# Performance work log

Hardware: AMD Instinct MI355X
Metric: run time of the kernel (lower is better)

Reference implementation:

```python
import jax, jax.numpy as jnp
import numpy as np
from jax import lax

EPS = 1e-5

def _bn(x):
    # BatchNorm1d, training-mode batch stats, affine at init (gamma=1, beta=0)
    return (x - x.mean(0)) / jnp.sqrt(x.var(0) + EPS)

def _nonlinear(x, W1, W2):
    h = jax.nn.relu(_bn(x @ W1.T))
    return jax.nn.relu(_bn(h @ W2.T))

def _conv_bn_lrelu(x, w):
    # x: [E, C, L], w: [O, C, 3], padding=1; BN over (batch, length)
    y = lax.conv_general_dilated(x, w, (1,), [(1, 1)], dimension_numbers=('NCH', 'OIH', 'NCH'))
    m = y.mean((0, 2), keepdims=True)
    v = y.var((0, 2), keepdims=True)
    y = (y - m) / jnp.sqrt(v + EPS)
    return jnp.where(y >= 0, y, 0.01 * y)  # LeakyReLU(negative_slope=0.01)

def _curve_encoder(x, c1, c2, c3, fc):
    y = _conv_bn_lrelu(x, c1)
    y = _conv_bn_lrelu(y, c2)
    y = _conv_bn_lrelu(y, c3)
    y = y.mean(-1)            # AdaptiveAvgPool1d(1)
    return _bn(y @ fc.T)      # _fc: Linear(bias=False) + BN, no activation

def _forward(attn_bias, angle, centroid_distance, edge_data, edge_type,
             edge_length, edge_convexity, node_feat,
             sd_emb, virt, angle_W1, angle_W2, cent_W1, cent_W2,
             etype_W1, etype_W2, elen_W1, elen_W2, econv_W1, econv_W2,
             curv_c1, curv_c2, curv_c3, curv_fc, edis_w,
             ec_Wp, ec_W1, ec_W2,
             shortest_distance, edge_path, edge_padding_mask, src, dst):
    B, N, _ = shortest_distance.shape
    H = sd_emb.shape[1]
    D = edge_path.shape[-1]           # multi_hop_max_dist
    n_edge = edge_padding_mask.shape[1]

    bias = jnp.broadcast_to(attn_bias[:, None], (B, H, N + 1, N + 1))

    # shortest-distance / angle / centroid biases, all [B, H, N, N]
    sdb = sd_emb[shortest_distance].transpose(0, 3, 1, 2)
    ang = _nonlinear(angle.reshape(-1, 1), angle_W1, angle_W2).reshape(B, N, N, H).transpose(0, 3, 1, 2)
    cen = _nonlinear(centroid_distance.reshape(-1, 1), cent_W1, cent_W2).reshape(B, N, N, H).transpose(0, 3, 1, 2)

    # --- multi_hop branch ---
    ef = (_curve_encoder(edge_data.transpose(0, 2, 1), curv_c1, curv_c2, curv_c3, curv_fc)
          + _nonlinear(edge_type, etype_W1, etype_W2)
          + _nonlinear(edge_length[:, None], elen_W1, elen_W2)
          + _nonlinear(edge_convexity, econv_W1, econv_W2))     # [E, H]
    # EdgeConv (UV-Net style node_cat): proj(n[src]) + proj(n[dst]) + efeat -> MLP -> BN -> ReLU
    proj = node_feat @ ec_Wp.T
    agg = proj[src] + proj[dst] + ef
    h = jax.nn.relu(_bn(agg @ ec_W1.T)) @ ec_W2.T
    ef2 = jax.nn.relu(_bn(h))                                   # [E, H]

    # edge_padding_mask is all-False, so edge_feature[edge_pos] = ef2 is a plain
    # row-major reshape; slot n_edge stays zero (padding target of edge_path)
    edge_feature = jnp.zeros((B, n_edge + 1, H), dtype=edge_data.dtype)
    edge_feature = edge_feature.at[:, :n_edge].set(ef2.reshape(B, n_edge, H))

    sd_ = jnp.where(shortest_distance == 0, 1, shortest_distance)
    sd_ = jnp.where(sd_ > 1, sd_ - 1, sd_)
    sd_ = jnp.clip(sd_, 0, D)

    ep = edge_path.reshape(B, N * N * D)
    eb = jnp.take_along_axis(edge_feature, ep[:, :, None], axis=1).reshape(B, N, N, D, H)
    Wd = edis_w.reshape(-1, H, H)[:D]                           # [D, H, H]
    eb = jnp.einsum('bijdh,dhk->bijk', eb, Wd)                  # per-hop bmm fused with hop-sum
    eb = eb / (sd_.astype(eb.dtype)[..., None] + 1e-6)
    eb = jnp.nan_to_num(eb)
    ebias = eb.transpose(0, 3, 1, 2)                            # [B, H, N, N]

    bias = bias.at[:, :, 1:, 1:].add(sdb + ang + cen + ebias)
    t = virt.reshape(1, H, 1)
    bias = bias.at[:, :, 1:, 0].add(t)
    bias = bias.at[:, :, 0, :].add(t)
    return bias + attn_bias[:, None]


def setup_inputs() -> dict:
    key = jax.random.key(0)
    ks = iter(jax.random.split(key, 48))
    B, N, H, D = 4, 256, 16, 5
    n_edge, n_pts = 1024, 20
    dim_node, num_distance, num_edge_dis = 256, 512, 128
    E = B * n_edge
    tot_nodes = B * N
    rn = lambda *s: jax.random.normal(next(ks), s, jnp.float32)
    return {
        'attn_bias': rn(B, N + 1, N + 1),
        'shortest_distance': jax.random.randint(next(ks), (B, N, N), 0, num_distance),
        'angle': rn(B, N, N),
        'centroid_distance': rn(B, N, N),
        'edge_path': jax.random.randint(next(ks), (B, N, N, D), 0, n_edge + 1),
        'edge_data': rn(E, n_pts, 12),
        'edge_type': rn(E, 11),
        'edge_length': rn(E),
        'edge_convexity': rn(E, 3),
        'edge_padding_mask': jnp.zeros((B, n_edge), dtype=bool),
        'src': jax.random.randint(next(ks), (E,), 0, tot_nodes),
        'dst': jax.random.randint(next(ks), (E,), 0, tot_nodes),
        'node_feat': rn(tot_nodes, dim_node),
        'sd_emb': (rn(num_distance, H) * 0.02).at[0].set(0.0),  # padding_idx=0
        'virt': rn(1, H) * 0.02,
        'angle_W1': rn(H, 1) * 0.1, 'angle_W2': rn(H, H) * 0.1,
        'cent_W1': rn(H, 1) * 0.1, 'cent_W2': rn(H, H) * 0.1,
        'etype_W1': rn(H, 11) * 0.1, 'etype_W2': rn(H, H) * 0.1,
        'elen_W1': rn(H, 1) * 0.1, 'elen_W2': rn(H, H) * 0.1,
        'econv_W1': rn(H, 3) * 0.1, 'econv_W2': rn(H, H) * 0.1,
        'curv_c1': rn(64, 12, 3) * 0.1, 'curv_c2': rn(128, 64, 3) * 0.05,
        'curv_c3': rn(256, 128, 3) * 0.05, 'curv_fc': rn(H, 256) * 0.05,
        'edis_w': rn(num_edge_dis * H * H, 1) * 0.02,
        'ec_Wp': rn(H, dim_node) * 0.02, 'ec_W1': rn(64, H) * 0.02, 'ec_W2': rn(H, 64) * 0.02,
    }


def reference(attn_bias, shortest_distance, angle, centroid_distance, edge_path,
              edge_data, edge_type, edge_length, edge_convexity, edge_padding_mask,
              src, dst, node_feat, sd_emb, virt, angle_W1, angle_W2, cent_W1, cent_W2,
              etype_W1, etype_W2, elen_W1, elen_W2, econv_W1, econv_W2,
              curv_c1, curv_c2, curv_c3, curv_fc, edis_w, ec_Wp, ec_W1, ec_W2):
    return _forward(attn_bias, angle, centroid_distance, edge_data, edge_type,
                    edge_length, edge_convexity, node_feat,
                    sd_emb, virt, angle_W1, angle_W2, cent_W1, cent_W2,
                    etype_W1, etype_W2, elen_W1, elen_W2, econv_W1, econv_W2,
                    curv_c1, curv_c2, curv_c3, curv_fc, edis_w,
                    ec_Wp, ec_W1, ec_W2,
                    shortest_distance, edge_path, edge_padding_mask, src, dst)
```

## Files before the change

### kernel.cpp

```cpp
#include <hip/hip_runtime.h>

#define EPSB 1e-5f
#define B_ 4
#define N_ 256
#define H_ 16
#define D_ 5
#define E_ 4096
#define M_PAIR (B_*N_*N_)

typedef __attribute__((ext_vector_type(8))) short short8;
typedef __attribute__((ext_vector_type(4))) float f32x4;

enum {
  SO_ANGX = 0,
  SO_CENX = 2,
  SO_MOMA = 16,
  SO_MOMC = 24,
  SO_C1   = 96,  SO_C1Q   = 160,
  SO_C2   = 224, SO_C2Q   = 352,
  SO_C3   = 480, SO_C3Q   = 736,
  SO_FC   = 992, SO_FCQ   = 1008,
  SO_ET1  = 1024, SO_ET1Q = 1040,
  SO_ET2  = 1056, SO_ET2Q = 1072,
  SO_EL1  = 1088, SO_EL1Q = 1104,
  SO_EL2  = 1120, SO_EL2Q = 1136,
  SO_EV1  = 1152, SO_EV1Q = 1168,
  SO_EV2  = 1184, SO_EV2Q = 1200,
  SO_G1   = 1216, SO_G1Q  = 1280,
  SO_G2   = 1344, SO_G2Q  = 1360,
  STATS_FLOATS = 2048
};

static constexpr size_t F_Y13  = 2048;
static constexpr size_t F_Y2   = F_Y13 + 10485760;
static constexpr size_t F_POOL = F_Y2 + 5242880;
static constexpr size_t F_FCB  = F_POOL + 1048576;
static constexpr size_t F_EF   = F_FCB + 65536;
static constexpr size_t F_PROJ = F_EF + 65536;
static constexpr size_t F_Z1EC = F_PROJ + 16384;
static constexpr size_t F_Z2T  = F_Z1EC + 262144;
static constexpr size_t F_G    = F_Z2T + 196608;
static constexpr size_t F_WT2  = F_G + 328000;
static constexpr size_t F_WT3  = F_WT2 + 12288;

__device__ __forceinline__ float waveSum(float v){
  #pragma unroll
  for(int o=32;o;o>>=1) v += __shfl_down(v,o);
  return v;
}

__device__ __forceinline__ ushort f2bf(float f){
  uint u = __float_as_uint(f);
  uint r = (u + 0x7FFF + ((u>>16)&1)) >> 16;
  return (ushort)r;
}
__device__ __forceinline__ float bf2f(ushort u){
  return __uint_as_float(((uint)u)<<16);
}

__device__ __forceinline__ void red32_atomic(float* ws, int so, int soq, float* s, float* q){
  __shared__ float red[4][32];
  int tid=threadIdx.x, lane=tid&63, wid=tid>>6;
  #pragma unroll
  for(int k=0;k<16;k++){
    float rs=waveSum(s[k]), rq=waveSum(q[k]);
    if(lane==0){ red[wid][k]=rs; red[wid][16+k]=rq; }
  }
  __syncthreads();
  if(tid<32){
    float t=red[0][tid]+red[1][tid]+red[2][tid]+red[3][tid];
    atomicAdd(&ws[tid<16 ? so+tid : soq+(tid-16)], t);
  }
}

__global__ __launch_bounds__(256) void k_conv1(const float* __restrict__ ed,
    const float* __restrict__ w, float* __restrict__ ws){
  __shared__ float wsh[64*37];
  __shared__ float xs[8*12*20];
  __shared__ float reds[256], redq[256];
  int tid=threadIdx.x;
  for(int i=tid;i<2304;i+=256){ int o=i/36, r=i%36; wsh[o*37+r]=w[i]; }
  int e0=blockIdx.x*8;
  for(int i=tid;i<1920;i+=256){
    int e=i/240, r=i%240, l=r/12, c=r%12;
    xs[(e*12+c)*20+l]=ed[(size_t)(e0+e)*240+r];
  }
  __syncthreads();
  int o=tid&63, eg=tid>>6;
  ushort* y1=(ushort*)(ws+F_Y13);
  float ssum=0, ssq=0;
  for(int ee=0;ee<2;ee++){
    int e=eg*2+ee;
    float acc[20];
    #pragma unroll
    for(int l=0;l<20;l++) acc[l]=0;
    for(int c=0;c<12;c++){
      float w0=wsh[o*37+c*3], w1=wsh[o*37+c*3+1], w2=wsh[o*37+c*3+2];
      const float* xr=xs+(e*12+c)*20;
      #pragma unroll
      for(int l=0;l<20;l++){
        acc[l]=fmaf(w1,xr[l],acc[l]);
        if(l>0)  acc[l]=fmaf(w0,xr[l-1],acc[l]);
        if(l<19) acc[l]=fmaf(w2,xr[l+1],acc[l]);
      }
    }
    size_t base=((size_t)(e0+e)*20)*64;
    #pragma unroll
    for(int l=0;l<20;l++){
      y1[base+(size_t)l*64+o]=f2bf(acc[l]);
      ssum+=acc[l]; ssq+=acc[l]*acc[l];
    }
  }
  reds[eg*64+o]=ssum; redq[eg*64+o]=ssq;
  __syncthreads();
  if(tid<64){
    atomicAdd(&ws[SO_C1+tid], reds[tid]+reds[64+tid]+reds[128+tid]+reds[192+tid]);
  } else if(tid<128){
    int oo=tid-64;
    atomicAdd(&ws[SO_C1Q+oo], redq[oo]+redq[64+oo]+redq[128+oo]+redq[192+oo]);
  }
}


__device__ void dev_wprep(int bid, const float* __restrict__ c2w,
    const float* __restrict__ c3w, ushort* __restrict__ wt2, ushort* __restrict__ wt3){
  int t = bid*256 + threadIdx.x;
  if(t < 128*192){
    int idx=t;
    int j=idx&7, lane=(idx>>3)&63, ks=(idx>>9)%6, ct=idx/3072;
    int l16=lane&15, lhi=lane>>4;
    int o=ct*16+l16, tap=ks/2, c=(ks%2)*32+lhi*8+j;
    wt2[idx]=f2bf(c2w[(o*64+c)*3+tap]);
  } else {
    int idx=t-128*192;
    if(idx<256*384){
      int j=idx&7, lane=(idx>>3)&63, ks=(idx>>9)%12, ct=idx/6144;
      int l16=lane&15, lhi=lane>>4;
      int o=ct*16+l16, tap=ks/4, c=(ks%4)*32+lhi*8+j;
      wt3[idx]=f2bf(c3w[(o*128+c)*3+tap]);
    }
  }
}

__device__ void dev_proj(int bid, const float* __restrict__ nf,
    const float* __restrict__ Wp, float* __restrict__ ws, char* pool){
  float* wps=(float*)pool;
  int tid=threadIdx.x;
  for(int i=tid;i<4096;i+=256){ wps[(i>>8)*260+(i&255)]=Wp[i]; }
  __syncthreads();
  int t=bid*256+tid;
  int v=t>>4, h=t&15;
  const float4* row=(const float4*)(nf+(size_t)v*256);
  const float4* wr=(const float4*)(wps+h*260);
  float z=0;
  #pragma unroll 8
  for(int c=0;c<64;c++){
    float4 a=row[c], b=wr[c];
    z+=a.x*b.x+a.y*b.y+a.z*b.z+a.w*b.w;
  }
  ws[F_PROJ+t]=z;
}

__device__ void dev_scalar(int bid, const float* __restrict__ ang,
    const float* __restrict__ cen, float* __restrict__ st){
  int tid = bid*256 + threadIdx.x;
  float sa=0, qa=0, sc=0, qc=0;
  for(int i=tid; i<M_PAIR; i += 256*256){
    float a=ang[i], c=cen[i];
    sa+=a; qa+=a*a; sc+=c; qc+=c*c;
  }
  __shared__ float red[4][4];
  int lane=threadIdx.x&63, wid=threadIdx.x>>6;
  sa=waveSum(sa); qa=waveSum(qa); sc=waveSum(sc); qc=waveSum(qc);
  if(lane==0){ red[wid][0]=sa; red[wid][1]=qa; red[wid][2]=sc; red[wid][3]=qc; }
  __syncthreads();
  if(threadIdx.x<4){
    float t=red[0][threadIdx.x]+red[1][threadIdx.x]+red[2][threadIdx.x]+red[3][threadIdx.x];
    atomicAdd(&st[threadIdx.x], t);
  }
}

template<int DIM>
__device__ void dev_sml1(const float* __restrict__ x,
    const float* __restrict__ W1, float* __restrict__ ws, int so, int soq, int bid){
  __shared__ float w1s[176];
  int tid=threadIdx.x;
  if(tid<16*DIM) w1s[tid]=W1[tid];
  __syncthreads();
  int e=bid*256+tid;
  float xv[DIM];
  #pragma unroll
  for(int j=0;j<DIM;j++) xv[j]=x[(size_t)e*DIM+j];
  float s[16], q[16];
  #pragma unroll
  for(int k=0;k<16;k++){
    float z=0;
    #pragma unroll
    for(int j=0;j<DIM;j++) z+=w1s[k*DIM+j]*xv[j];
    s[k]=z; q[k]=z*z;
  }
  red32_atomic(ws, so, soq, s, q);
}

__global__ __launch_bounds__(256) void k_misc(
    const float* __restrict__ c2w, const float* __restrict__ c3w,
    const float* __restrict__ nf, const float* __restrict__ Wp,
    const float* __restrict__ ang, const float* __restrict__ cen,
    const float* __restrict__ et, const float* __restrict__ el, const float* __restrict__ ev,
    const float* __restrict__ etW1, const float* __restrict__ elW1, const float* __restrict__ evW1,
    float* __restrict__ ws){
  __shared__ char pool[16640];
  int bx=blockIdx.x;
  if(bx<480)       dev_wprep(bx, c2w, c3w, (ushort*)(ws+F_WT2), (ushort*)(ws+F_WT3));
  else if(bx<544)  dev_proj(bx-480, nf, Wp, ws, pool);
  else if(bx<800)  dev_scalar(bx-544, ang, cen, ws);
  else {
    int bid=bx-800;
    int g=bid>>4, b2=bid&15;
    if(g==0)      dev_sml1<11>(et,etW1,ws,SO_ET1,SO_ET1Q,b2);
    else if(g==1) dev_sml1<1> (el,elW1,ws,SO_EL1,SO_EL1Q,b2);
    else          dev_sml1<3> (ev,evW1,ws,SO_EV1,SO_EV1Q,b2);
  }
}


__device__ void dev_mom2(int bid, const float* __restrict__ x, float* __restrict__ st,
    int soX, int mo){
  int tid=threadIdx.x;
  float mu = st[soX]*(1.0f/262144.0f);
  float P=0,N=0,Pq=0,Nq=0;
  for(int i=bid*256+tid; i<M_PAIR; i+=32*256){
    float dx=x[i]-mu;
    if(dx>0){ P+=dx; Pq+=dx*dx; } else { N+=dx; Nq+=dx*dx; }
  }
  __shared__ float red[4][4];
  int lane=tid&63, wid=tid>>6;
  P=waveSum(P); N=waveSum(N); Pq=waveSum(Pq); Nq=waveSum(Nq);
  if(lane==0){ red[wid][0]=P; red[wid][1]=N; red[wid][2]=Pq; red[wid][3]=Nq; }
  __syncthreads();
  if(tid<4){
    float t=red[0][tid]+red[1][tid]+red[2][tid]+red[3][tid];
    atomicAdd(&st[mo+tid], t);
  }
}

template<int DIM>
__device__ void dev_sml2(const float* __restrict__ x,
    const float* __restrict__ W1, const float* __restrict__ W2,
    float* __restrict__ ws, int so1, int so1q, int so2, int so2q,
    float* __restrict__ z2out, int bid){
  __shared__ float w1s[176];
  __shared__ float w2s[256];
  __shared__ float mi[16][2];
  int tid=threadIdx.x;
  if(tid<16*DIM) w1s[tid]=W1[tid];
  w2s[tid]=W2[tid];
  if(tid<16){
    float m=ws[so1+tid]*(1.0f/4096.0f);
    float v=ws[so1q+tid]*(1.0f/4096.0f)-m*m; if(v<0)v=0;
    mi[tid][0]=m; mi[tid][1]=rsqrtf(v+EPSB);
  }
  __syncthreads();
  int e=bid*256+tid;
  float xv[DIM];
  #pragma unroll
  for(int j=0;j<DIM;j++) xv[j]=x[(size_t)e*DIM+j];
  float h1[16];
  #pragma unroll
  for(int h=0;h<16;h++){
    float z=0;
    #pragma unroll
    for(int j=0;j<DIM;j++) z+=w1s[h*DIM+j]*xv[j];
    z=(z-mi[h][0])*mi[h][1];
    h1[h]=z>0?z:0;
  }
  float s[16], q[16];
  #pragma unroll
  for(int k=0;k<16;k++){
    float z=0;
    #pragma unroll
    for(int h=0;h<16;h++) z+=w2s[k*16+h]*h1[h];
    z2out[(size_t)e*16+k]=z;
    s[k]=z; q[k]=z*z;
  }
  red32_atomic(ws, so2, so2q, s, q);
}

__global__ __launch_bounds__(256) void k_stats2(
    const float* __restrict__ ang, const float* __restrict__ cen,
    const float* __restrict__ et, const float* __restrict__ el, const float* __restrict__ ev,
    const float* __restrict__ etW1, const float* __restrict__ etW2,
    const float* __restrict__ elW1, const float* __restrict__ elW2,
    const float* __restrict__ evW1, const float* __restrict__ evW2,
    float* __restrict__ ws){
  int bx=blockIdx.x;
  if(bx<32)       dev_mom2(bx, ang, ws, SO_ANGX, SO_MOMA);
  else if(bx<64)  dev_mom2(bx-32, cen, ws, SO_CENX, SO_MOMC);
  else {
    int bid=bx-64;
    int g=bid>>4, b2=bid&15;
    if(g==0)      dev_sml2<11>(et,etW1,etW2,ws,SO_ET1,SO_ET1Q,SO_ET2,SO_ET2Q,ws+F_Z2T,b2);
    else if(g==1) dev_sml2<1> (el,elW1,elW2,ws,SO_EL1,SO_EL1Q,SO_EL2,SO_EL2Q,ws+F_Z2T+65536,b2);
    else          dev_sml2<3> (ev,evW1,evW2,ws,SO_EV1,SO_EV1Q,SO_EV2,SO_EV2Q,ws+F_Z2T+131072,b2);
  }
}

template<int CIN, int OUT, int EPB, int NSPLIT>
__global__ __launch_bounds__(256) void k_convmf(
    const ushort* __restrict__ yin, const ushort* __restrict__ wt,
    ushort* __restrict__ yout, float* __restrict__ ws,
    int soIn, int soInQ, int soOut, int soOutQ)
{
  constexpr int K = CIN*3;
  constexpr int KSTEPS = K/32;
  constexpr int M = EPB*20;
  constexpr int ROWT = M/16;
  constexpr int ROWS = EPB*22;
  constexpr int RB = CIN*2;
  constexpr uint SWZ = RB/16 - 1;
  __shared__ ushort xs[ROWS*CIN];
  __shared__ float mi[CIN][2];
  int tid = threadIdx.x;
  int bx = blockIdx.x;
  int eblk = bx / NSPLIT, split = bx % NSPLIT;
  int lane = tid&63, wid = tid>>6;
  int l16 = lane&15, lhi = lane>>4;
  int colbase = (split*4 + wid) * 16;

  const ushort* wp = wt + ((size_t)(colbase>>4)*KSTEPS)*512 + (size_t)lane*8;
  short8 bF[KSTEPS];
  #pragma unroll
  for(int ks=0;ks<KSTEPS;ks++) bF[ks]=*(const short8*)(wp + (size_t)ks*512);

  for(int c=tid; c<CIN; c+=256){
    float m=ws[soIn+c]*(1.0f/81920.0f);
    float v=ws[soInQ+c]*(1.0f/81920.0f)-m*m; if(v<0)v=0;
    mi[c][0]=m; mi[c][1]=rsqrtf(v+EPSB);
  }
  uint* xs32 = (uint*)xs;
  for(int i=tid; i<EPB*2*(CIN/2); i+=256){
    int e=i/(CIN), r=i%(CIN); int lp = (r < CIN/2)? 0:21; int cw = r%(CIN/2);
    xs32[(e*22+lp)*(CIN/2)+cw]=0;
  }
  __syncthreads();
  int e0 = eblk*EPB;
  const ushort* src = yin + (size_t)e0*20*CIN;
  for(int i=tid; i<EPB*20*(CIN/8); i+=256){
    int c8 = i%(CIN/8); int rl = i/(CIN/8);
    int c = c8*8;
    short8 v = *(const short8*)(src + (size_t)rl*CIN + c);
    uint pk[4];
    #pragma unroll
    for(int jj=0;jj<4;jj++){
      float f0 = bf2f((ushort)v[jj*2]);
      float f1 = bf2f((ushort)v[jj*2+1]);
      f0=(f0-mi[c+jj*2  ][0])*mi[c+jj*2  ][1]; f0= f0>=0?f0:0.01f*f0;
      f1=(f1-mi[c+jj*2+1][0])*mi[c+jj*2+1][1]; f1= f1>=0?f1:0.01f*f1;
      pk[jj] = (uint)f2bf(f0) | ((uint)f2bf(f1)<<16);
    }
    int e = rl/20, l=rl%20;
    int row = e*22 + l + 1;
    uint byteoff = (uint)row*RB + (((uint)c*2) ^ (uint)((row&SWZ)<<4));
    *(uint4*)((char*)xs + byteoff) = make_uint4(pk[0],pk[1],pk[2],pk[3]);
  }
  __syncthreads();

  f32x4 acc[ROWT];
  #pragma unroll
  for(int m=0;m<ROWT;m++) acc[m]=(f32x4){0,0,0,0};
  int rowc[ROWT];
  #pragma unroll
  for(int m=0;m<ROWT;m++){ int r=m*16+l16; rowc[m]=(r/20)*22 + (r%20); }

  short8 aF0[ROWT], aF1[ROWT];

#define LOADA(ksv, A) { \
    int t_=(ksv)/(CIN/32); int c0_=((ksv)%(CIN/32))*32 + lhi*8; \
    _Pragma("unroll") \
    for(int m=0;m<ROWT;m++){ \
      int row_=rowc[m]+t_; \
      uint off_=(uint)row_*RB + (((uint)c0_*2) ^ (uint)((row_&SWZ)<<4)); \
      A[m]=*(const short8*)((char*)xs+off_); } }

#define MFMAK(A, ksv) { \
    _Pragma("unroll") \
    for(int m=0;m<ROWT;m++) \
      acc[m]=__builtin_amdgcn_mfma_f32_16x16x32_bf16(A[m],bF[ksv],acc[m],0,0,0); }

  LOADA(0, aF0);
  #pragma unroll
  for(int kp=0; kp<KSTEPS/2; kp++){
    LOADA(kp*2+1, aF1);
    MFMAK(aF0, kp*2);
    if(kp*2+2<KSTEPS) LOADA(kp*2+2, aF0);
    MFMAK(aF1, kp*2+1);
  }
#undef LOADA
#undef MFMAK

  {
    float s=0,q=0;
    #pragma unroll
    for(int m=0;m<ROWT;m++)
      #pragma unroll
      for(int j=0;j<4;j++){ float a=acc[m][j]; s+=a; q+=a*a; }
    s += __shfl_xor(s,16); s += __shfl_xor(s,32);
    q += __shfl_xor(q,16); q += __shfl_xor(q,32);
    if(lhi==0){
      int o = colbase+l16;
      atomicAdd(&ws[soOut+o], s);
      atomicAdd(&ws[soOutQ+o], q);
    }
  }
  ushort* dst = yout + (size_t)eblk*M*OUT;
  #pragma unroll
  for(int m=0;m<ROWT;m++)
    #pragma unroll
    for(int j=0;j<4;j++){
      int R = m*16 + lhi*4 + j;
      dst[(size_t)R*OUT + colbase + l16] = f2bf(acc[m][j]);
    }
}

__global__ __launch_bounds__(256) void k_poolfc(const float* __restrict__ fcw, float* __restrict__ ws){
  __shared__ float ps[16][260];
  __shared__ float red[4][32];
  __shared__ float mo[256][2];
  int tid=threadIdx.x;
  {
    float m=ws[SO_C3+tid]*(1.0f/81920.0f);
    float v=ws[SO_C3Q+tid]*(1.0f/81920.0f)-m*m; if(v<0)v=0;
    mo[tid][0]=m; mo[tid][1]=rsqrtf(v+EPSB);
  }
  __syncthreads();
  int e0=blockIdx.x*16;
  const ushort* y3=(const ushort*)(ws+F_Y13);
  float m=mo[tid][0], inv=mo[tid][1];
  for(int el=0;el<16;el++){
    const ushort* row=y3+((size_t)(e0+el)*20)*256+tid;
    float s=0;
    #pragma unroll
    for(int l=0;l<20;l++){
      float x=(bf2f(row[(size_t)l*256])-m)*inv;
      s += x>=0.f? x : 0.01f*x;
    }
    ps[el][tid]=s*(1.0f/20.0f);
  }
  __syncthreads();
  int e=tid>>4, h=tid&15;
  const float* wr=fcw+(size_t)h*256;
  float z=0;
  for(int c=0;c<256;c++) z+=ps[e][c]*wr[c];
  ws[F_FCB+(size_t)(e0+e)*16+h]=z;
  float s=z, q=z*z;
  #pragma unroll
  for(int o=16;o<64;o<<=1){ s+=__shfl_down(s,o); q+=__shfl_down(q,o); }
  int lane=tid&63, wid=tid>>6;
  if(lane<16){ red[wid][lane]=s; red[wid][16+lane]=q; }
  __syncthreads();
  if(tid<32){
    float v=red[0][tid]+red[1][tid]+red[2][tid]+red[3][tid];
    atomicAdd(&ws[tid<16? SO_FC+tid : SO_FCQ+(tid-16)], v);
  }
}

__device__ __constant__ int EF_BASES[4][2] = {
  {SO_ET2,SO_ET2Q},{SO_EL2,SO_EL2Q},{SO_EV2,SO_EV2Q},{SO_FC,SO_FCQ}
};

__global__ __launch_bounds__(256) void k_aggef(const int* __restrict__ src, const int* __restrict__ dst,
    const float* __restrict__ ecW1, float* __restrict__ ws){
  __shared__ float w1s[64*17];
  __shared__ float mi[4][16][2];
  __shared__ float aLDS[32][17];
  __shared__ float zLDS[64][33];
  __shared__ float reds[4][64], redq[4][64];
  int tid=threadIdx.x;
  for(int i=tid;i<1024;i+=256) w1s[(i>>4)*17+(i&15)]=ecW1[i];
  if(tid<64){
    int g=tid>>4, h=tid&15;
    float m=ws[EF_BASES[g][0]+h]*(1.0f/4096.0f);
    float v=ws[EF_BASES[g][1]+h]*(1.0f/4096.0f)-m*m; if(v<0)v=0;
    mi[g][h][0]=m; mi[g][h][1]=rsqrtf(v+EPSB);
  }
  __syncthreads();
  int e0=blockIdx.x*32;
  for(int it=tid; it<32*16; it+=256){
    int el=it>>4, h=it&15;
    int e=e0+el;
    float z=ws[F_FCB+(size_t)e*16+h];
    float a=(z-mi[3][h][0])*mi[3][h][1];
    #pragma unroll
    for(int g=0;g<3;g++){
      float z2=ws[F_Z2T+(size_t)g*65536+(size_t)e*16+h];
      float r=(z2-mi[g][h][0])*mi[g][h][1];
      a+= r>0?r:0;
    }
    int s=src[e], d=dst[e];
    a+=ws[F_PROJ+(size_t)s*16+h]+ws[F_PROJ+(size_t)d*16+h];
    aLDS[el][h]=a;
  }
  __syncthreads();
  int o=tid&63, elq=tid>>6;
  float s=0,q=0;
  #pragma unroll
  for(int j=0;j<8;j++){
    int el=elq*8+j;
    float z=0;
    #pragma unroll
    for(int h=0;h<16;h++) z+=w1s[o*17+h]*aLDS[el][h];
    zLDS[o][el]=z;
    s+=z; q+=z*z;
  }
  reds[elq][o]=s; redq[elq][o]=q;
  __syncthreads();
  for(int idx=tid; idx<2048; idx+=256){
    int oo=idx>>5, el=idx&31;
    ws[F_Z1EC+(size_t)oo*E_+e0+el]=zLDS[oo][el];
  }
  if(tid<64){
    atomicAdd(&ws[SO_G1+tid], reds[0][tid]+reds[1][tid]+reds[2][tid]+reds[3][tid]);
  } else if(tid<128){
    int oo=tid-64;
    atomicAdd(&ws[SO_G1Q+oo], redq[0][oo]+redq[1][oo]+redq[2][oo]+redq[3][oo]);
  }
}

__global__ __launch_bounds__(256) void k_ec2(const float* __restrict__ ecW2, float* __restrict__ ws){
  __shared__ float w2s[1024];
  __shared__ float mi[64][2];
  int tid=threadIdx.x;
  for(int i=tid;i<1024;i+=256) w2s[i]=ecW2[i];
  if(tid<64){
    float m=ws[SO_G1+tid]*(1.0f/4096.0f);
    float v=ws[SO_G1Q+tid]*(1.0f/4096.0f)-m*m; if(v<0)v=0;
    mi[tid][0]=m; mi[tid][1]=rsqrtf(v+EPSB);
  }
  __syncthreads();
  int el=tid&63, kq=tid>>6;
  int e=blockIdx.x*64+el;
  float acc[4]={0,0,0,0};
  #pragma unroll 8
  for(int o=0;o<64;o++){
    float z=ws[F_Z1EC+(size_t)o*E_+e];
    float h=(z-mi[o][0])*mi[o][1];
    h=h>0?h:0;
    #pragma unroll
    for(int j=0;j<4;j++) acc[j]+=w2s[(kq*4+j)*64+o]*h;
  }
  #pragma unroll
  for(int j=0;j<4;j++) ws[F_FCB+(size_t)e*16+kq*4+j]=acc[j];
  #pragma unroll
  for(int j=0;j<4;j++){
    float rs=waveSum(acc[j]);
    float rq=waveSum(acc[j]*acc[j]);
    if(el==0){
      atomicAdd(&ws[SO_G2+kq*4+j], rs);
      atomicAdd(&ws[SO_G2Q+kq*4+j], rq);
    }
  }
}

__global__ __launch_bounds__(256) void k_ef2g(const float* __restrict__ edisw, float* __restrict__ ws){
  __shared__ float wd[1280];
  __shared__ float mi[16][2];
  int tid=threadIdx.x;
  for(int i=tid;i<1280;i+=256) wd[i]=edisw[i];
  if(tid<16){
    float m=ws[SO_G2+tid]*(1.0f/4096.0f);
    float va=ws[SO_G2Q+tid]*(1.0f/4096.0f)-m*m; if(va<0)va=0;
    mi[tid][0]=m; mi[tid][1]=rsqrtf(va+EPSB);
  }
  __syncthreads();
  int t=blockIdx.x*256+tid;
  if(t>=4*1025*5) return;
  int bp=t/5, d=t%5;
  int b=bp/1025, pos=bp%1025;
  float ef[16];
  if(pos<1024){
    int e=b*1024+pos;
    #pragma unroll
    for(int k=0;k<16;k++){
      float z=ws[F_FCB+(size_t)e*16+k];
      float v=(z-mi[k][0])*mi[k][1];
      ef[k]= v>0?v:0;
    }
  } else {
    #pragma unroll
    for(int k=0;k<16;k++) ef[k]=0;
  }
  float* g=ws+F_G+(size_t)bp*80+d*16;
  const float* wdd=wd+d*256;
  #pragma unroll
  for(int k=0;k<16;k++){
    float s=0;
    #pragma unroll
    for(int h=0;h<16;h++) s+=ef[h]*wdd[h*16+k];
    g[k]=s;
  }
}

__global__ __launch_bounds__(256) void k_pair(const float* __restrict__ ab,
    const int* __restrict__ sd, const float* __restrict__ ang, const float* __restrict__ cen,
    const int* __restrict__ ep, const float* __restrict__ sdemb,
    const float* __restrict__ angW1, const float* __restrict__ angW2,
    const float* __restrict__ cenW1, const float* __restrict__ cenW2,
    const float* __restrict__ ws, float* __restrict__ out){
  __shared__ float cpa[16],cma[16],m2a[16],i2a[16];
  __shared__ float cpc[16],cmc[16],m2c[16],i2c[16];
  __shared__ float mv[4];
  int tid=threadIdx.x;
  if(tid==0){
    float s=ws[SO_ANGX], q=ws[SO_ANGX+1];
    float mu=s*(1.0f/262144.0f);
    float v=q*(1.0f/262144.0f)-mu*mu; if(v<0)v=0;
    mv[0]=mu; mv[1]=v;
    s=ws[SO_CENX]; q=ws[SO_CENX+1];
    mu=s*(1.0f/262144.0f);
    v=q*(1.0f/262144.0f)-mu*mu; if(v<0)v=0;
    mv[2]=mu; mv[3]=v;
  }
  __syncthreads();
  if(tid<32){
    int k=tid&15; bool isC = tid>=16;
    const float* W1=isC?cenW1:angW1; const float* W2=isC?cenW2:angW2;
    float var=isC?mv[3]:mv[1];
    float cp=0, cm=0;
    for(int h=0;h<16;h++){
      float w=W1[h];
      float A=w*rsqrtf(var*w*w+EPSB);
      float wk=W2[k*16+h];
      if(A>0) cp+=wk*A; else cm+=wk*A;
    }
    int mo = isC? SO_MOMC : SO_MOMA;
    float P=ws[mo], N=ws[mo+1], Pq=ws[mo+2], Nq=ws[mo+3];
    float mean=(cp*P+cm*N)*(1.0f/262144.0f);
    float e2=(cp*cp*Pq+cm*cm*Nq)*(1.0f/262144.0f);
    float v2=e2-mean*mean; if(v2<0)v2=0;
    float iv=rsqrtf(v2+EPSB);
    if(!isC){ cpa[k]=cp; cma[k]=cm; m2a[k]=mean; i2a[k]=iv; }
    else    { cpc[k]=cp; cmc[k]=cm; m2c[k]=mean; i2c[k]=iv; }
  }
  __syncthreads();
  int t=blockIdx.x*256+tid;
  int b=t>>16, rem=t&65535, i=rem>>8, j=rem&255;
  int sdv=sd[t];
  float xa=ang[t], xc0=cen[t];
  float acc[16];
  const float* se=sdemb+(size_t)sdv*16;
  #pragma unroll
  for(int k=0;k<16;k++) acc[k]=se[k];
  {
    float dx=xa-mv[0];
    bool pos=dx>0.f;
    #pragma unroll
    for(int k=0;k<16;k++){
      float z=dx*(pos?cpa[k]:cma[k]);
      float r=(z-m2a[k])*i2a[k];
      acc[k]+= r>0?r:0;
    }
  }
  {
    float dx=xc0-mv[2];
    bool pos=dx>0.f;
    #pragma unroll
    for(int k=0;k<16;k++){
      float z=dx*(pos?cpc[k]:cmc[k]);
      float r=(z-m2c[k])*i2c[k];
      acc[k]+= r>0?r:0;
    }
  }
  {
    int sdm = sdv==0 ? 1 : sdv;
    if(sdm>1) sdm-=1;
    if(sdm>5) sdm=5;
    float inv=1.0f/((float)sdm+1e-6f);
    float eb[16];
    #pragma unroll
    for(int k=0;k<16;k++) eb[k]=0;
    const float* G=ws+F_G;
    #pragma unroll
    for(int d=0;d<5;d++){
      int idx=ep[(size_t)t*5+d];
      const float4* g=(const float4*)(G+(size_t)(b*1025+idx)*80+d*16);
      float4 g0=g[0], g1=g[1], g2=g[2], g3=g[3];
      eb[0]+=g0.x; eb[1]+=g0.y; eb[2]+=g0.z; eb[3]+=g0.w;
      eb[4]+=g1.x; eb[5]+=g1.y; eb[6]+=g1.z; eb[7]+=g1.w;
      eb[8]+=g2.x; eb[9]+=g2.y; eb[10]+=g2.z; eb[11]+=g2.w;
      eb[12]+=g3.x; eb[13]+=g3.y; eb[14]+=g3.z; eb[15]+=g3.w;
    }
    #pragma unroll
    for(int k=0;k<16;k++) acc[k]+=eb[k]*inv;
  }
  float base2=2.0f*ab[(size_t)b*66049+(size_t)(i+1)*257+(j+1)];
  #pragma unroll
  for(int k=0;k<16;k++)
    out[(((size_t)b*16+k)*257+(i+1))*257+(j+1)]=acc[k]+base2;
}

__global__ __launch_bounds__(256) void k_border(const float* __restrict__ ab,
    const float* __restrict__ virt, float* __restrict__ out){
  int t=blockIdx.x*256+threadIdx.x;
  if(t>=4*16*513) return;
  int idx=t%513, bh=t/513;
  int b=bh>>4, h=bh&15;
  float v=virt[h];
  if(idx<257){
    out[(((size_t)b*16+h)*257)*257+idx]=2.0f*ab[(size_t)b*66049+idx]+v;
  } else {
    int p=idx-256;
    out[(((size_t)b*16+h)*257+p)*257]=2.0f*ab[(size_t)b*66049+(size_t)p*257]+v;
  }
}

extern "C" void kernel_launch(void* const* d_in, const int* in_sizes, int n_in,
                              void* d_out, int out_size, void* d_ws, size_t ws_size,
                              hipStream_t stream) {
  const float* ab    =(const float*)d_in[0];
  const int*   sdist =(const int*)  d_in[1];
  const float* ang   =(const float*)d_in[2];
  const float* cen   =(const float*)d_in[3];
  const int*   ep    =(const int*)  d_in[4];
  const float* edata =(const float*)d_in[5];
  const float* etype =(const float*)d_in[6];
  const float* elen  =(const float*)d_in[7];
  const float* econv =(const float*)d_in[8];
  const int*   src   =(const int*)  d_in[10];
  const int*   dst   =(const int*)  d_in[11];
  const float* nf    =(const float*)d_in[12];
  const float* sdemb =(const float*)d_in[13];
  const float* virt  =(const float*)d_in[14];
  const float* angW1 =(const float*)d_in[15];
  const float* angW2 =(const float*)d_in[16];
  const float* cenW1 =(const float*)d_in[17];
  const float* cenW2 =(const float*)d_in[18];
  const float* etW1  =(const float*)d_in[19];
  const float* etW2  =(const float*)d_in[20];
  const float* elW1  =(const float*)d_in[21];
  const float* elW2  =(const float*)d_in[22];
  const float* evW1  =(const float*)d_in[23];
  const float* evW2  =(const float*)d_in[24];
  const float* c1w   =(const float*)d_in[25];
  const float* c2w   =(const float*)d_in[26];
  const float* c3w   =(const float*)d_in[27];
  const float* fcw   =(const float*)d_in[28];
  const float* edisw =(const float*)d_in[29];
  const float* ecWp  =(const float*)d_in[30];
  const float* ecW1  =(const float*)d_in[31];
  const float* ecW2  =(const float*)d_in[32];
  float* ws=(float*)d_ws;
  float* out=(float*)d_out;

  hipMemsetAsync(d_ws, 0, STATS_FLOATS*sizeof(float), stream);

  k_conv1<<<512,256,0,stream>>>(edata,c1w,ws);
  k_misc<<<848,256,0,stream>>>(c2w,c3w,nf,ecWp,ang,cen,
                               etype,elen,econv,etW1,elW1,evW1,ws);
  k_stats2<<<112,256,0,stream>>>(ang,cen,etype,elen,econv,
                                 etW1,etW2,elW1,elW2,evW1,evW2,ws);

  k_convmf<64,128,4,2><<<2048,256,0,stream>>>((const ushort*)(ws+F_Y13),(const ushort*)(ws+F_WT2),
                                              (ushort*)(ws+F_Y2),ws,SO_C1,SO_C1Q,SO_C2,SO_C2Q);
  k_convmf<128,256,4,4><<<4096,256,0,stream>>>((const ushort*)(ws+F_Y2),(const ushort*)(ws+F_WT3),
                                               (ushort*)(ws+F_Y13),ws,SO_C2,SO_C2Q,SO_C3,SO_C3Q);
  k_poolfc<<<256,256,0,stream>>>(fcw,ws);

  k_aggef<<<128,256,0,stream>>>(src,dst,ecW1,ws);
  k_ec2<<<64,256,0,stream>>>(ecW2,ws);
  k_ef2g<<<81,256,0,stream>>>(edisw,ws);

  k_pair<<<1024,256,0,stream>>>(ab,sdist,ang,cen,ep,sdemb,angW1,angW2,cenW1,cenW2,ws,out);
  k_border<<<129,256,0,stream>>>(ab,virt,out);
}
```

Baseline: 207.0 us.

## Give each wave multiple output column tiles in conv MFMA kernel, pad LDS rows

The conv MFMA kernel now has each wave compute several 16-wide output column tiles (WCOLT), reusing each loaded A fragment across them. For the third conv this halves the number of blocks and the redundant LDS staging and BN-apply work done per block. The XOR swizzle on LDS rows is replaced by a 16-byte row padding to avoid bank conflicts. The cost is more accumulator and B-fragment registers per thread, which may lower occupancy, and there are fewer blocks to spread across the GPU.

```diff
diff --git a/kernel.cpp b/kernel.cpp
--- a/kernel.cpp
+++ b/kernel.cpp
@@ -315,32 +315,36 @@
   constexpr int KSTEPS = K/32;
   constexpr int M = EPB*20;
   constexpr int ROWT = M/16;
+  constexpr int WCOLT = OUT/(64*NSPLIT);
   constexpr int ROWS = EPB*22;
-  constexpr int RB = CIN*2;
-  constexpr uint SWZ = RB/16 - 1;
-  __shared__ ushort xs[ROWS*CIN];
+  constexpr int RBp = CIN*2 + 16;
+  constexpr int RWp = RBp/4;
+  __shared__ char xsb[ROWS*RBp];
   __shared__ float mi[CIN][2];
   int tid = threadIdx.x;
   int bx = blockIdx.x;
   int eblk = bx / NSPLIT, split = bx % NSPLIT;
   int lane = tid&63, wid = tid>>6;
   int l16 = lane&15, lhi = lane>>4;
-  int colbase = (split*4 + wid) * 16;
-
-  const ushort* wp = wt + ((size_t)(colbase>>4)*KSTEPS)*512 + (size_t)lane*8;
-  short8 bF[KSTEPS];
-  #pragma unroll
-  for(int ks=0;ks<KSTEPS;ks++) bF[ks]=*(const short8*)(wp + (size_t)ks*512);
+  int colbase = (split*4 + wid) * (OUT/(4*NSPLIT));
+
+  short8 bF[WCOLT][KSTEPS];
+  #pragma unroll
+  for(int n=0;n<WCOLT;n++){
+    const ushort* wp = wt + ((size_t)(colbase/16 + n)*KSTEPS)*512 + (size_t)lane*8;
+    #pragma unroll
+    for(int ks=0;ks<KSTEPS;ks++) bF[n][ks]=*(const short8*)(wp + (size_t)ks*512);
+  }
 
   for(int c=tid; c<CIN; c+=256){
     float m=ws[soIn+c]*(1.0f/81920.0f);
     float v=ws[soInQ+c]*(1.0f/81920.0f)-m*m; if(v<0)v=0;
     mi[c][0]=m; mi[c][1]=rsqrtf(v+EPSB);
   }
-  uint* xs32 = (uint*)xs;
+  uint* xs32 = (uint*)xsb;
   for(int i=tid; i<EPB*2*(CIN/2); i+=256){
     int e=i/(CIN), r=i%(CIN); int lp = (r < CIN/2)? 0:21; int cw = r%(CIN/2);
-    xs32[(e*22+lp)*(CIN/2)+cw]=0;
+    xs32[(e*22+lp)*RWp+cw]=0;
   }
   __syncthreads();
   int e0 = eblk*EPB;
@@ -360,14 +364,15 @@
     }
     int e = rl/20, l=rl%20;
     int row = e*22 + l + 1;
-    uint byteoff = (uint)row*RB + (((uint)c*2) ^ (uint)((row&SWZ)<<4));
-    *(uint4*)((char*)xs + byteoff) = make_uint4(pk[0],pk[1],pk[2],pk[3]);
-  }
-  __syncthreads();
-
-  f32x4 acc[ROWT];
-  #pragma unroll
-  for(int m=0;m<ROWT;m++) acc[m]=(f32x4){0,0,0,0};
+    *(uint4*)(xsb + (size_t)row*RBp + c*2) = make_uint4(pk[0],pk[1],pk[2],pk[3]);
+  }
+  __syncthreads();
+
+  f32x4 acc[ROWT][WCOLT];
+  #pragma unroll
+  for(int m=0;m<ROWT;m++)
+    #pragma unroll
+    for(int n=0;n<WCOLT;n++) acc[m][n]=(f32x4){0,0,0,0};
   int rowc[ROWT];
   #pragma unroll
   for(int m=0;m<ROWT;m++){ int r=m*16+l16; rowc[m]=(r/20)*22 + (r%20); }
@@ -379,13 +384,14 @@
     _Pragma("unroll") \
     for(int m=0;m<ROWT;m++){ \
       int row_=rowc[m]+t_; \
-      uint off_=(uint)row_*RB + (((uint)c0_*2) ^ (uint)((row_&SWZ)<<4)); \
-      A[m]=*(const short8*)((char*)xs+off_); } }
+      A[m]=*(const short8*)(xsb + (size_t)row_*RBp + c0_*2); } }
 
 #define MFMAK(A, ksv) { \
     _Pragma("unroll") \
     for(int m=0;m<ROWT;m++) \
-      acc[m]=__builtin_amdgcn_mfma_f32_16x16x32_bf16(A[m],bF[ksv],acc[m],0,0,0); }
+      _Pragma("unroll") \
+      for(int n=0;n<WCOLT;n++) \
+        acc[m][n]=__builtin_amdgcn_mfma_f32_16x16x32_bf16(A[m],bF[n][ksv],acc[m][n],0,0,0); }
 
   LOADA(0, aF0);
   #pragma unroll
@@ -398,16 +404,17 @@
 #undef LOADA
 #undef MFMAK
 
-  {
+  #pragma unroll
+  for(int n=0;n<WCOLT;n++){
     float s=0,q=0;
     #pragma unroll
     for(int m=0;m<ROWT;m++)
       #pragma unroll
-      for(int j=0;j<4;j++){ float a=acc[m][j]; s+=a; q+=a*a; }
+      for(int j=0;j<4;j++){ float a=acc[m][n][j]; s+=a; q+=a*a; }
     s += __shfl_xor(s,16); s += __shfl_xor(s,32);
     q += __shfl_xor(q,16); q += __shfl_xor(q,32);
     if(lhi==0){
-      int o = colbase+l16;
+      int o = colbase+n*16+l16;
       atomicAdd(&ws[soOut+o], s);
       atomicAdd(&ws[soOutQ+o], q);
     }
@@ -418,7 +425,9 @@
     #pragma unroll
     for(int j=0;j<4;j++){
       int R = m*16 + lhi*4 + j;
-      dst[(size_t)R*OUT + colbase + l16] = f2bf(acc[m][j]);
+      #pragma unroll
+      for(int n=0;n<WCOLT;n++)
+        dst[(size_t)R*OUT + colbase + n*16 + l16] = f2bf(acc[m][n][j]);
     }
 }
 
@@ -761,7 +770,7 @@
 
   k_convmf<64,128,4,2><<<2048,256,0,stream>>>((const ushort*)(ws+F_Y13),(const ushort*)(ws+F_WT2),
                                               (ushort*)(ws+F_Y2),ws,SO_C1,SO_C1Q,SO_C2,SO_C2Q);
-  k_convmf<128,256,4,4><<<4096,256,0,stream>>>((const ushort*)(ws+F_Y2),(const ushort*)(ws+F_WT3),
+  k_convmf<128,256,4,2><<<2048,256,0,stream>>>((const ushort*)(ws+F_Y2),(const ushort*)(ws+F_WT3),
                                                (ushort*)(ws+F_Y13),ws,SO_C2,SO_C2Q,SO_C3,SO_C3Q);
   k_poolfc<<<256,256,0,stream>>>(fcw,ws);
 
```

After: 205.3 us. Within noise of the previous version (-0.8%).
